# Performance work log

Measured on AMD Instinct MI355X. Metric: run time of the kernel, lower is better.

The kernel has to match this reference:

```python
import jax, jax.numpy as jnp
import numpy as np

TOKENS, D_MODEL, VOCAB, K = 4096, 1024, 32000, 128


def setup_inputs() -> dict:
    key = jax.random.key(0)
    k1, k2 = jax.random.split(key)
    x = jax.random.normal(k1, (TOKENS, D_MODEL), dtype=jnp.float32)
    proj_weight = jax.random.normal(k2, (VOCAB, D_MODEL), dtype=jnp.float32)
    return {"x": x, "proj_weight": proj_weight, "k": K}


def reference(x, proj_weight, k):
    # faiss.knn_gpu with default METRIC_L2: squared L2 distances, k smallest.
    x_sq = jnp.sum(x * x, axis=-1, keepdims=True)            # [tokens, 1]
    b_sq = jnp.sum(proj_weight * proj_weight, axis=-1)        # [vocab]
    dots = jnp.einsum("td,vd->tv", x, proj_weight)           # [tokens, vocab]
    dist = x_sq - 2.0 * dots + b_sq[None, :]                  # [tokens, vocab]
    neg_vals, _ = jax.lax.top_k(-dist, k)                     # k smallest distances
    D = -neg_vals                                             # [tokens, k]
    return D
```

## Files before the change

kernel.cpp:

```cpp
#include <hip/hip_runtime.h>
#include <stdint.h>

#define TOKENS 4096
#define DMODEL 1024
#define VOCAB  32000
#define KSEL   128

#define BM 128
#define BN 128
#define BK 64

#define NB  2048
#define CAP 2048

typedef __attribute__((ext_vector_type(8))) short short8;
typedef __attribute__((ext_vector_type(4))) float f32x4;

__device__ __forceinline__ unsigned short f2bf(float f) {
  uint32_t u = __float_as_uint(f);
  uint32_t r = (u + 0x7fffu + ((u >> 16) & 1u)) >> 16;
  return (unsigned short)r;
}
__device__ __forceinline__ unsigned encf(float f) {
  unsigned u = __float_as_uint(f);
  return (u >> 31) ? ~u : (u | 0x80000000u);
}
__device__ __forceinline__ float decf(unsigned e) {
  return __uint_as_float((e >> 31) ? (e & 0x7fffffffu) : ~e);
}

__global__ __launch_bounds__(256)
void conv_rows(const float* __restrict__ src, unsigned short* __restrict__ dst,
               float* __restrict__ sq, int nrows) {
  int row = blockIdx.x;
  int t = threadIdx.x;
  const float4* s4 = (const float4*)(src + (size_t)row * DMODEL);
  float4 v = s4[t];
  float ss = v.x*v.x + v.y*v.y + v.z*v.z + v.w*v.w;
  uint2 pk;
  pk.x = (uint32_t)f2bf(v.x) | ((uint32_t)f2bf(v.y) << 16);
  pk.y = (uint32_t)f2bf(v.z) | ((uint32_t)f2bf(v.w) << 16);
  ((uint2*)(dst + (size_t)row * DMODEL))[t] = pk;

  __shared__ float red[256];
  red[t] = ss; __syncthreads();
  for (int s = 128; s > 0; s >>= 1) {
    if (t < s) red[t] += red[t + s];
    __syncthreads();
  }
  if (t == 0) sq[row] = red[0];
}

__global__ __launch_bounds__(256)
void gemm_dist(const unsigned short* __restrict__ Xb,
               const unsigned short* __restrict__ Wb,
               const float* __restrict__ xsq, const float* __restrict__ bsq,
               unsigned short* __restrict__ dist,
               unsigned* __restrict__ rminE, unsigned* __restrict__ rmaxE,
               int row0) {
  __shared__ unsigned short As[BM * BK];
  __shared__ unsigned short Bs[BN * BK];
  __shared__ unsigned rminS[BM], rmaxS[BM];

  int tid  = threadIdx.x;
  int lane = tid & 63;
  int wid  = tid >> 6;
  int wr   = wid >> 1;
  int wc   = wid & 1;

  int nwg = gridDim.x * gridDim.y;
  int bid = blockIdx.y * gridDim.x + blockIdx.x;
  int cpx = nwg >> 3;
  int o   = (bid & 7) * cpx + (bid >> 3);
  int NR  = gridDim.y;
  int GR  = (NR & 3) ? 1 : 4;
  int span = gridDim.x * GR;
  int sg  = o / span;
  int rem = o - sg * span;
  int bn  = rem / GR;
  int bm  = sg * GR + (rem - bn * GR);

  int rowBase = row0 + bm * BM;
  int colBase = bn * BN;

  for (int i = tid; i < BM; i += 256) { rminS[i] = 0xFFFFFFFFu; rmaxS[i] = 0u; }

  f32x4 acc[4][4];
#pragma unroll
  for (int m = 0; m < 4; m++)
#pragma unroll
    for (int n = 0; n < 4; n++) acc[m][n] = (f32x4){0.f, 0.f, 0.f, 0.f};

  const unsigned short* Ag = Xb + (size_t)rowBase * DMODEL;
  const unsigned short* Bg = Wb + (size_t)colBase * DMODEL;

  int r16 = lane & 15;
  int kg  = lane >> 4;

  for (int kt = 0; kt < DMODEL; kt += BK) {
#pragma unroll
    for (int c = 0; c < 4; c++) {
      int g   = (c * 4 + wid) * 64 + lane;
      int r   = g >> 3;
      int col = (g & 7) * 8;
      const unsigned short* ga = Ag + (size_t)r * DMODEL + kt + col;
      const unsigned short* gb = Bg + (size_t)r * DMODEL + kt + col;
      int chunkElems = (c * 4 + wid) * 512;
      __builtin_amdgcn_global_load_lds(
          (const __attribute__((address_space(1))) void*)ga,
          (__attribute__((address_space(3))) void*)(&As[chunkElems]), 16, 0, 0);
      __builtin_amdgcn_global_load_lds(
          (const __attribute__((address_space(1))) void*)gb,
          (__attribute__((address_space(3))) void*)(&Bs[chunkElems]), 16, 0, 0);
    }
    __syncthreads();

#pragma unroll
    for (int kk = 0; kk < BK; kk += 32) {
      short8 a[4], b[4];
#pragma unroll
      for (int m = 0; m < 4; m++)
        a[m] = *(const short8*)&As[(wr * 64 + m * 16 + r16) * BK + kk + kg * 8];
#pragma unroll
      for (int n = 0; n < 4; n++)
        b[n] = *(const short8*)&Bs[(wc * 64 + n * 16 + r16) * BK + kk + kg * 8];
#pragma unroll
      for (int m = 0; m < 4; m++)
#pragma unroll
        for (int n = 0; n < 4; n++)
          acc[m][n] = __builtin_amdgcn_mfma_f32_16x16x32_bf16(a[m], b[n], acc[m][n], 0, 0, 0);
    }
    __syncthreads();
  }

  int col16 = lane & 15;
  int rg    = lane >> 4;
  float bq[4];
#pragma unroll
  for (int n = 0; n < 4; n++) bq[n] = bsq[colBase + wc * 64 + n * 16 + col16];

#pragma unroll
  for (int m = 0; m < 4; m++) {
#pragma unroll
    for (int i = 0; i < 4; i++) {
      int lrow = wr * 64 + m * 16 + rg * 4 + i;
      int rowL = bm * BM + lrow;
      float xq = xsq[row0 + rowL];
      float mn = 3.4e38f, mx = -3.4e38f;
#pragma unroll
      for (int n = 0; n < 4; n++) {
        float d = xq + bq[n] - 2.0f * acc[m][n][i];
        unsigned short h = f2bf(d);
        float dr = __uint_as_float((unsigned)h << 16);
        dist[(size_t)rowL * VOCAB + colBase + wc * 64 + n * 16 + col16] = h;
        mn = fminf(mn, dr);
        mx = fmaxf(mx, dr);
      }
      atomicMin(&rminS[lrow], encf(mn));
      atomicMax(&rmaxS[lrow], encf(mx));
    }
  }
  __syncthreads();
  if (tid < BM) {
    atomicMin(&rminE[row0 + bm * BM + tid], rminS[tid]);
    atomicMax(&rmaxE[row0 + bm * BM + tid], rmaxS[tid]);
  }
}

__device__ __forceinline__ int binOf(float x, float mn, float invw) {
  int b = (int)((x - mn) * invw);
  b = b < 0 ? 0 : b;
  return b < NB - 1 ? b : NB - 1;
}

__device__ __forceinline__ void scanFind(unsigned* bins, unsigned* s_scan,
                                         unsigned target, int* s_B,
                                         unsigned* s_cum, int t) {
  unsigned ssum = 0;
  int base = t * (NB / 256);
#pragma unroll
  for (int j = 0; j < NB / 256; j++) ssum += bins[base + j];
  s_scan[t] = ssum;
  __syncthreads();
  for (int off = 1; off < 256; off <<= 1) {
    unsigned add = (t >= off) ? s_scan[t - off] : 0u;
    __syncthreads();
    s_scan[t] += add;
    __syncthreads();
  }
  unsigned incl = s_scan[t];
  unsigned excl = incl - ssum;
  if (excl < target && incl >= target) {
    unsigned cum = excl;
    for (int j = 0; j < NB / 256; j++) {
      cum += bins[base + j];
      if (cum >= target) { *s_B = base + j; *s_cum = cum; break; }
    }
  }
  __syncthreads();
}

__global__ __launch_bounds__(256)
void select_topk(const unsigned short* __restrict__ dist,
                 const unsigned* __restrict__ rminE,
                 const unsigned* __restrict__ rmaxE,
                 float* __restrict__ out, int row0) {
  int r = blockIdx.x;
  int t = threadIdx.x;
  int grow = row0 + r;
  const unsigned short* rowp = dist + (size_t)r * VOCAB;

  __shared__ unsigned s_scan[256];
  __shared__ unsigned bins[NB];
  __shared__ float    cand[CAP];
  __shared__ unsigned s_cnt;
  __shared__ int      s_B;
  __shared__ unsigned s_cum;

  float rmn = decf(rminE[grow]);
  float rmx = decf(rmaxE[grow]);
  float range = rmx - rmn;

  if (!(range > 1e-20f)) {
    for (int i = t; i < KSEL; i += 256)
      out[(size_t)grow * KSEL + i] = rmn;
    return;
  }
  float invw = (float)NB / range;

  for (int i = t; i < NB; i += 256) bins[i] = 0;
  __syncthreads();
  const uint4* rp4 = (const uint4*)rowp;
  for (int i = t; i < VOCAB / 8; i += 256) {
    uint4 u = rp4[i];
    unsigned w[4] = {u.x, u.y, u.z, u.w};
#pragma unroll
    for (int j = 0; j < 4; j++) {
      float lo = __uint_as_float(w[j] << 16);
      float hi = __uint_as_float(w[j] & 0xffff0000u);
      atomicAdd(&bins[binOf(lo, rmn, invw)], 1u);
      atomicAdd(&bins[binOf(hi, rmn, invw)], 1u);
    }
  }
  __syncthreads();

  scanFind(bins, s_scan, KSEL, &s_B, &s_cum, t);
  int B = s_B;

  if (t == 0) s_cnt = 0;
  __syncthreads();
  for (int i = t; i < VOCAB / 8; i += 256) {
    uint4 u = rp4[i];
    unsigned w[4] = {u.x, u.y, u.z, u.w};
#pragma unroll
    for (int j = 0; j < 4; j++) {
#pragma unroll
      for (int h = 0; h < 2; h++) {
        float x = __uint_as_float(h ? (w[j] & 0xffff0000u) : (w[j] << 16));
        if (binOf(x, rmn, invw) <= B) {
          unsigned idx = atomicAdd(&s_cnt, 1u);
          if (idx < CAP) cand[idx] = x;
        }
      }
    }
  }
  __syncthreads();
  int m = (int)(s_cnt < CAP ? s_cnt : CAP);

  for (int i = t; i < m; i += 256) {
    float vi = cand[i];
    int rk = 0;
    for (int j = 0; j < m; j++) {
      float vj = cand[j];
      rk += (vj < vi) || (vj == vi && j < i);
    }
    if (rk < KSEL) out[(size_t)grow * KSEL + rk] = vi;
  }
}

extern "C" void kernel_launch(void* const* d_in, const int* in_sizes, int n_in,
                              void* d_out, int out_size, void* d_ws, size_t ws_size,
                              hipStream_t stream) {
  const float* x = (const float*)d_in[0];
  const float* w = (const float*)d_in[1];
  float* out = (float*)d_out;

  char* ws = (char*)d_ws;
  size_t off = 0;
  auto alloc = [&](size_t bytes) -> char* {
    off = (off + 255) & ~(size_t)255;
    char* p = ws + off;
    off += bytes;
    return p;
  };
  unsigned short* Xb = (unsigned short*)alloc((size_t)TOKENS * DMODEL * 2);
  unsigned short* Wb = (unsigned short*)alloc((size_t)VOCAB * DMODEL * 2);
  float* xsq = (float*)alloc((size_t)TOKENS * 4);
  float* bsq = (float*)alloc((size_t)VOCAB * 4);
  unsigned* rminE = (unsigned*)alloc((size_t)TOKENS * 4);
  unsigned* rmaxE = (unsigned*)alloc((size_t)TOKENS * 4);
  off = (off + 255) & ~(size_t)255;
  size_t fixed = off;

  int TS = TOKENS;
  while (TS > 128 && fixed + (size_t)TS * VOCAB * 2 > ws_size) TS >>= 1;
  unsigned short* dist = (unsigned short*)(ws + fixed);

  hipMemsetAsync(rminE, 0xFF, (size_t)TOKENS * 4, stream);
  hipMemsetAsync(rmaxE, 0x00, (size_t)TOKENS * 4, stream);

  conv_rows<<<TOKENS, 256, 0, stream>>>(x, Xb, xsq, TOKENS);
  conv_rows<<<VOCAB, 256, 0, stream>>>(w, Wb, bsq, VOCAB);

  for (int row0 = 0; row0 < TOKENS; row0 += TS) {
    dim3 g(VOCAB / BN, TS / BM);
    gemm_dist<<<g, 256, 0, stream>>>(Xb, Wb, xsq, bsq, dist, rminE, rmaxE, row0);
    select_topk<<<TS, 256, 0, stream>>>(dist, rminE, rmaxE, out, row0);
  }
}
```

Measured before the change: 801.8 us.

## Stage distance tile in LDS for coalesced stores; use global min/max range

The GEMM epilogue now writes bf16 distances into a swizzled shared-memory tile and then copies it to global memory as 16-byte coalesced stores, replacing scattered 2-byte stores. Per-row min/max tracking with shared atomics is replaced by a wave-shuffle reduction into a single global min/max used by every row for histogram binning. This removes the per-row atomics, but each row's histogram range is now wider, so more candidates may fall into the threshold bin. The chunk size is also capped at 2048 rows, which means two GEMM/select passes.

```diff
diff --git a/kernel.cpp b/kernel.cpp
--- a/kernel.cpp
+++ b/kernel.cpp
@@ -56,11 +56,12 @@
                const unsigned short* __restrict__ Wb,
                const float* __restrict__ xsq, const float* __restrict__ bsq,
                unsigned short* __restrict__ dist,
-               unsigned* __restrict__ rminE, unsigned* __restrict__ rmaxE,
+               unsigned* __restrict__ gmnE, unsigned* __restrict__ gmxE,
                int row0) {
-  __shared__ unsigned short As[BM * BK];
-  __shared__ unsigned short Bs[BN * BK];
-  __shared__ unsigned rminS[BM], rmaxS[BM];
+  __shared__ unsigned short S[BM * BK * 2];
+  unsigned short* As = S;
+  unsigned short* Bs = S + BM * BK;
+  __shared__ unsigned wmn[4], wmx[4];
 
   int tid  = threadIdx.x;
   int lane = tid & 63;
@@ -82,8 +83,6 @@
 
   int rowBase = row0 + bm * BM;
   int colBase = bn * BN;
-
-  for (int i = tid; i < BM; i += 256) { rminS[i] = 0xFFFFFFFFu; rmaxS[i] = 0u; }
 
   f32x4 acc[4][4];
 #pragma unroll
@@ -139,31 +138,50 @@
 #pragma unroll
   for (int n = 0; n < 4; n++) bq[n] = bsq[colBase + wc * 64 + n * 16 + col16];
 
+  float mnT = 3.4e38f, mxT = -3.4e38f;
 #pragma unroll
   for (int m = 0; m < 4; m++) {
 #pragma unroll
     for (int i = 0; i < 4; i++) {
-      int lrow = wr * 64 + m * 16 + rg * 4 + i;
-      int rowL = bm * BM + lrow;
-      float xq = xsq[row0 + rowL];
-      float mn = 3.4e38f, mx = -3.4e38f;
+      int row = wr * 64 + m * 16 + rg * 4 + i;
+      float xq = xsq[rowBase + row];
 #pragma unroll
       for (int n = 0; n < 4; n++) {
         float d = xq + bq[n] - 2.0f * acc[m][n][i];
         unsigned short h = f2bf(d);
         float dr = __uint_as_float((unsigned)h << 16);
-        dist[(size_t)rowL * VOCAB + colBase + wc * 64 + n * 16 + col16] = h;
-        mn = fminf(mn, dr);
-        mx = fmaxf(mx, dr);
+        mnT = fminf(mnT, dr);
+        mxT = fmaxf(mxT, dr);
+        int col = wc * 64 + n * 16 + col16;
+        int byte = (row << 8) + (col << 1);
+        byte ^= (row & 12) << 3;
+        *(unsigned short*)((char*)S + byte) = h;
       }
-      atomicMin(&rminS[lrow], encf(mn));
-      atomicMax(&rmaxS[lrow], encf(mx));
-    }
-  }
-  __syncthreads();
-  if (tid < BM) {
-    atomicMin(&rminE[row0 + bm * BM + tid], rminS[tid]);
-    atomicMax(&rmaxE[row0 + bm * BM + tid], rmaxS[tid]);
+    }
+  }
+#pragma unroll
+  for (int off = 32; off; off >>= 1) {
+    mnT = fminf(mnT, __shfl_xor(mnT, off));
+    mxT = fmaxf(mxT, __shfl_xor(mxT, off));
+  }
+  if (lane == 0) { wmn[wid] = encf(mnT); wmx[wid] = encf(mxT); }
+  __syncthreads();
+  if (tid == 0) {
+    unsigned a = min(min(wmn[0], wmn[1]), min(wmn[2], wmn[3]));
+    unsigned b = max(max(wmx[0], wmx[1]), max(wmx[2], wmx[3]));
+    atomicMin(gmnE, a);
+    atomicMax(gmxE, b);
+  }
+
+  size_t gbase = (size_t)(bm * BM) * VOCAB + colBase;
+#pragma unroll
+  for (int c = 0; c < 8; c++) {
+    int g   = c * 256 + tid;
+    int row = g >> 4;
+    int byte = (row << 8) + ((g & 15) << 4);
+    byte ^= (row & 12) << 3;
+    uint4 v = *(const uint4*)((const char*)S + byte);
+    *(uint4*)(dist + gbase + (size_t)row * VOCAB + ((g & 15) << 3)) = v;
   }
 }
 
@@ -202,8 +220,8 @@
 
 __global__ __launch_bounds__(256)
 void select_topk(const unsigned short* __restrict__ dist,
-                 const unsigned* __restrict__ rminE,
-                 const unsigned* __restrict__ rmaxE,
+                 const unsigned* __restrict__ gmnE,
+                 const unsigned* __restrict__ gmxE,
                  float* __restrict__ out, int row0) {
   int r = blockIdx.x;
   int t = threadIdx.x;
@@ -217,8 +235,8 @@
   __shared__ int      s_B;
   __shared__ unsigned s_cum;
 
-  float rmn = decf(rminE[grow]);
-  float rmx = decf(rmaxE[grow]);
+  float rmn = decf(gmnE[0]);
+  float rmx = decf(gmxE[0]);
   float range = rmx - rmn;
 
   if (!(range > 1e-20f)) {
@@ -297,24 +315,24 @@
   unsigned short* Wb = (unsigned short*)alloc((size_t)VOCAB * DMODEL * 2);
   float* xsq = (float*)alloc((size_t)TOKENS * 4);
   float* bsq = (float*)alloc((size_t)VOCAB * 4);
-  unsigned* rminE = (unsigned*)alloc((size_t)TOKENS * 4);
-  unsigned* rmaxE = (unsigned*)alloc((size_t)TOKENS * 4);
+  unsigned* gmnE = (unsigned*)alloc(4);
+  unsigned* gmxE = (unsigned*)alloc(4);
   off = (off + 255) & ~(size_t)255;
   size_t fixed = off;
 
-  int TS = TOKENS;
+  int TS = 2048;
   while (TS > 128 && fixed + (size_t)TS * VOCAB * 2 > ws_size) TS >>= 1;
   unsigned short* dist = (unsigned short*)(ws + fixed);
 
-  hipMemsetAsync(rminE, 0xFF, (size_t)TOKENS * 4, stream);
-  hipMemsetAsync(rmaxE, 0x00, (size_t)TOKENS * 4, stream);
+  hipMemsetAsync(gmnE, 0xFF, 4, stream);
+  hipMemsetAsync(gmxE, 0x00, 4, stream);
 
   conv_rows<<<TOKENS, 256, 0, stream>>>(x, Xb, xsq, TOKENS);
   conv_rows<<<VOCAB, 256, 0, stream>>>(w, Wb, bsq, VOCAB);
 
   for (int row0 = 0; row0 < TOKENS; row0 += TS) {
     dim3 g(VOCAB / BN, TS / BM);
-    gemm_dist<<<g, 256, 0, stream>>>(Xb, Wb, xsq, bsq, dist, rminE, rmaxE, row0);
-    select_topk<<<TS, 256, 0, stream>>>(dist, rminE, rmaxE, out, row0);
-  }
-}
+    gemm_dist<<<g, 256, 0, stream>>>(Xb, Wb, xsq, bsq, dist, gmnE, gmxE, row0);
+    select_topk<<<TS, 256, 0, stream>>>(dist, gmnE, gmxE, out, row0);
+  }
+}
```

New measurement: 750.3 us. 6.4% less time.
